# Kernel tuning notes

Measured on AMD Instinct MI355X. Metric: run time of the kernel, lower is better.

Reference implementation:

```python
import jax, jax.numpy as jnp
import numpy as np

V = 6890            # FAUST mesh vertices (also n_classes of the dense head)
C_IN = 3            # raw xyz signal
R, A = 5, 8         # kernel_size = (n_radial, n_angular)
ROT_DELTA = 1
ROTS = tuple(range(0, A, ROT_DELTA))  # 8 rotations
DIMS = [100, 100, 100]
EPS_BN = 1e-3       # keras BatchNormalization default epsilon


def setup_inputs() -> dict:
    key = jax.random.key(0)
    ks = jax.random.split(key, 12)
    inp = {}
    inp["signal"] = jax.random.normal(ks[0], (V, C_IN), jnp.float32)
    inp["bc_idx"] = jax.random.randint(ks[1], (V, R, A, 3), 0, V, dtype=jnp.int32)
    w = jax.random.uniform(ks[2], (V, R, A, 3), jnp.float32)
    inp["bc_w"] = w / jnp.sum(w, axis=-1, keepdims=True)  # convex barycentric weights
    # keras Normalization (not adapted): mean=0, var=1
    inp["norm_mean"] = jnp.zeros((C_IN,), jnp.float32)
    inp["norm_var"] = jnp.ones((C_IN,), jnp.float32)
    # ConvDirac templates: (amt_templates, n_radial, n_angular, c_in) + bias
    cins = [C_IN] + DIMS[:-1]
    for i, (ci, t) in enumerate(zip(cins, DIMS)):
        inp[f"w{i}"] = jax.random.normal(ks[3 + i], (t, R, A, ci), jnp.float32) * 0.05
        inp[f"b{i}"] = jnp.zeros((t,), jnp.float32)
    # BatchNorm (inference mode) params, stacked over the 3 blocks
    inp["bn_gamma"] = jnp.ones((3, DIMS[0]), jnp.float32)
    inp["bn_beta"] = jnp.zeros((3, DIMS[0]), jnp.float32)
    inp["bn_mean"] = jax.random.normal(ks[6], (3, DIMS[0]), jnp.float32) * 0.01
    inp["bn_var"] = jnp.ones((3, DIMS[0]), jnp.float32)
    inp["dense_w"] = jax.random.normal(ks[7], (DIMS[-1], V), jnp.float32) * 0.02
    inp["dense_b"] = jnp.zeros((V,), jnp.float32)
    return inp


def _isc_dirac(sig, bc_idx, bc_w, W, b):
    """Intrinsic surface conv (Dirac): barycentric patch gather + multi-rotation fold.
    sig: (V, C); bc_idx/bc_w: (V, R, A, 3); W: (T, R, A, C); b: (T,)
    returns (V, n_rot, T) after relu."""
    # patch operator: interpolate signal at template vertices -> (V, R, A, C)
    patch = jnp.einsum('vraic,vrai->vrac', sig[bc_idx], bc_w)
    # rotate the (small) template over the angular axis instead of the patch
    Wrot = jnp.stack([jnp.roll(W, -r, axis=2) for r in ROTS])  # (n_rot, T, R, A, C)
    out = jnp.einsum('vrac,ntrac->vnt', patch, Wrot) + b
    return jax.nn.relu(out)


def _amp(x):
    """AngularMaxPooling: keep the rotation response with max L2 norm. x: (V, n_rot, T)."""
    idx = jnp.argmax(jnp.linalg.norm(x, axis=-1), axis=-1)  # (V,)
    return jnp.take_along_axis(x, idx[:, None, None], axis=1)[:, 0, :]


def _bn(x, g, b, m, v):
    return g * (x - m) * jax.lax.rsqrt(v + EPS_BN) + b


def reference(signal, bc_idx, bc_w, norm_mean, norm_var, w0, b0, w1, b1, w2, b2,
              bn_gamma, bn_beta, bn_mean, bn_var, dense_w, dense_b):
    x = (signal - norm_mean) / jnp.sqrt(norm_var)
    for i, (W, b) in enumerate(((w0, b0), (w1, b1), (w2, b2))):
        x = _isc_dirac(x, bc_idx, bc_w, W, b)      # (V, n_rot, T)
        x = _amp(x)                                 # (V, T)
        x = _bn(x, bn_gamma[i], bn_beta[i], bn_mean[i], bn_var[i])
        # dropout: identity at inference
    return x @ dense_w + dense_b                    # (V, 6890)
```

## Files before the change

kernel.cpp:

```cpp
#include <hip/hip_runtime.h>

#define VN 6890
#define TN 100
#define NOUT 800
#define MP 6912
#define NP 896

typedef __attribute__((ext_vector_type(8))) short bf16x8;
typedef __attribute__((ext_vector_type(4))) float f32x4;

__device__ __forceinline__ unsigned short f2bf(float f) {
    unsigned u = __float_as_uint(f);
    return (unsigned short)((u + 0x7FFFu + ((u >> 16) & 1u)) >> 16);
}
__device__ __forceinline__ void split_bf16(float f, short* h, short* l) {
    unsigned short hb = f2bf(f);
    float hf = __uint_as_float(((unsigned)hb) << 16);
    *h = (short)hb;
    *l = (short)f2bf(f - hf);
}
__device__ __forceinline__ void gload16(const short* g, void* lds) {
    __builtin_amdgcn_global_load_lds(
        (const __attribute__((address_space(1))) void*)g,
        (__attribute__((address_space(3))) void*)lds, 16, 0, 0);
}

__global__ __launch_bounds__(256) void norm_kernel(
    const float* __restrict__ sig, const float* __restrict__ mean,
    const float* __restrict__ var, float* __restrict__ x0)
{
    int i = blockIdx.x * blockDim.x + threadIdx.x;
    if (i < VN * 3) {
        int c = i % 3;
        x0[i] = (sig[i] - mean[c]) / sqrtf(var[c]);
    }
}

template<int CIN, int KPAD>
__global__ __launch_bounds__(256) void rotw_split(
    const float* __restrict__ W, short* __restrict__ Bh, short* __restrict__ Bl)
{
    const int n = blockIdx.x;
    const int K = 40 * CIN;
    const int rot = n / TN, t = n - rot * TN;
    for (int k = threadIdx.x; k < KPAD; k += 256) {
        float w = 0.f;
        if (n < NOUT && k < K) {
            int ra = k / CIN, c = k - ra * CIN;
            int r = ra >> 3, a = ra & 7;
            int a2 = (a + rot) & 7;
            w = W[((t * 5 + r) * 8 + a2) * CIN + c];
        }
        short h, l; split_bf16(w, &h, &l);
        Bh[(size_t)n * KPAD + k] = h;
        Bl[(size_t)n * KPAD + k] = l;
    }
}

template<int CIN, int KPAD>
__global__ __launch_bounds__(256) void patch_split(
    const float* __restrict__ x, const int* __restrict__ bidx,
    const float* __restrict__ bw, short* __restrict__ Ph, short* __restrict__ Pl)
{
    __shared__ int   sIdx[120];
    __shared__ float sW[120];
    const int v = blockIdx.x;
    const int tid = threadIdx.x;
    const int K = 40 * CIN;
    if (v >= VN) {
        for (int e = tid; e < KPAD; e += 256) {
            Ph[(size_t)v * KPAD + e] = 0;
            Pl[(size_t)v * KPAD + e] = 0;
        }
        return;
    }
    if (tid < 120) { sIdx[tid] = bidx[v * 120 + tid]; sW[tid] = bw[v * 120 + tid]; }
    __syncthreads();
    for (int e = tid; e < KPAD; e += 256) {
        float s = 0.f;
        if (e < K) {
            int ra = e / CIN, c = e - ra * CIN;
            s = sW[ra * 3 + 0] * x[sIdx[ra * 3 + 0] * CIN + c]
              + sW[ra * 3 + 1] * x[sIdx[ra * 3 + 1] * CIN + c]
              + sW[ra * 3 + 2] * x[sIdx[ra * 3 + 2] * CIN + c];
        }
        short h, l; split_bf16(s, &h, &l);
        Ph[(size_t)v * KPAD + e] = h;
        Pl[(size_t)v * KPAD + e] = l;
    }
}

template<bool CONV_EPI>
__global__ __launch_bounds__(256, 2) void mfma_gemm(
    const short* __restrict__ Ah, const short* __restrict__ Al,
    const short* __restrict__ Bh, const short* __restrict__ Bl,
    const float* __restrict__ bias, float* __restrict__ C,
    int M, int N, int ldc, int K)
{
    __shared__ __align__(16) short AhS[4096];
    __shared__ __align__(16) short AlS[4096];
    __shared__ __align__(16) short BhS[4096];
    __shared__ __align__(16) short BlS[4096];

    const int tid  = threadIdx.x;
    const int wave = tid >> 6;
    const int lane = tid & 63;
    const int lr = lane & 15, lg = lane >> 4;
    const int wm = wave >> 1, wn = wave & 1;
    const int m0 = blockIdx.x * 128;
    const int n0 = blockIdx.y * 128;

    const int off0 = tid * 16, off1 = off0 + 4096;
    const int row0 = off0 >> 6, row1 = off1 >> 6;
    const int g0 = ((off0 >> 4) & 3) ^ ((row0 >> 1) & 3);
    const int g1 = ((off1 >> 4) & 3) ^ ((row1 >> 1) & 3);
    const size_t aO0 = (size_t)(m0 + row0) * K + g0 * 8;
    const size_t aO1 = (size_t)(m0 + row1) * K + g1 * 8;
    const size_t bO0 = (size_t)(n0 + row0) * K + g0 * 8;
    const size_t bO1 = (size_t)(n0 + row1) * K + g1 * 8;
    const int wofs = wave << 10;

    int aRd[4], bRd[4];
    #pragma unroll
    for (int f = 0; f < 4; ++f) {
        int ar = wm * 64 + f * 16 + lr;
        aRd[f] = ar * 64 + ((lg ^ ((ar >> 1) & 3)) << 4);
        int br = wn * 64 + f * 16 + lr;
        bRd[f] = br * 64 + ((lg ^ ((br >> 1) & 3)) << 4);
    }

    f32x4 acc[4][4];
    #pragma unroll
    for (int i = 0; i < 4; ++i)
        #pragma unroll
        for (int j = 0; j < 4; ++j)
            acc[i][j] = (f32x4){0.f, 0.f, 0.f, 0.f};

    const int nkt = K >> 5;
    for (int kt = 0; kt < nkt; ++kt) {
        const int k0 = kt << 5;
        gload16(Ah + aO0 + k0, (char*)AhS + wofs);
        gload16(Ah + aO1 + k0, (char*)AhS + 4096 + wofs);
        gload16(Al + aO0 + k0, (char*)AlS + wofs);
        gload16(Al + aO1 + k0, (char*)AlS + 4096 + wofs);
        gload16(Bh + bO0 + k0, (char*)BhS + wofs);
        gload16(Bh + bO1 + k0, (char*)BhS + 4096 + wofs);
        gload16(Bl + bO0 + k0, (char*)BlS + wofs);
        gload16(Bl + bO1 + k0, (char*)BlS + 4096 + wofs);
        __syncthreads();

        bf16x8 ah[4], al[4], bh[4], bl[4];
        #pragma unroll
        for (int f = 0; f < 4; ++f) {
            ah[f] = *(const bf16x8*)((const char*)AhS + aRd[f]);
            al[f] = *(const bf16x8*)((const char*)AlS + aRd[f]);
            bh[f] = *(const bf16x8*)((const char*)BhS + bRd[f]);
            bl[f] = *(const bf16x8*)((const char*)BlS + bRd[f]);
        }
        #pragma unroll
        for (int i = 0; i < 4; ++i)
            #pragma unroll
            for (int j = 0; j < 4; ++j)
                acc[i][j] = __builtin_amdgcn_mfma_f32_16x16x32_bf16(ah[i], bh[j], acc[i][j], 0, 0, 0);
        #pragma unroll
        for (int i = 0; i < 4; ++i)
            #pragma unroll
            for (int j = 0; j < 4; ++j)
                acc[i][j] = __builtin_amdgcn_mfma_f32_16x16x32_bf16(ah[i], bl[j], acc[i][j], 0, 0, 0);
        #pragma unroll
        for (int i = 0; i < 4; ++i)
            #pragma unroll
            for (int j = 0; j < 4; ++j)
                acc[i][j] = __builtin_amdgcn_mfma_f32_16x16x32_bf16(al[i], bh[j], acc[i][j], 0, 0, 0);
        __syncthreads();
    }

    #pragma unroll
    for (int i = 0; i < 4; ++i) {
        const int mb = m0 + wm * 64 + i * 16 + lg * 4;
        #pragma unroll
        for (int j = 0; j < 4; ++j) {
            const int n = n0 + wn * 64 + j * 16 + lr;
            if (CONV_EPI) {
                const float bv = bias[n % TN];
                #pragma unroll
                for (int q = 0; q < 4; ++q)
                    C[(size_t)(mb + q) * ldc + n] = fmaxf(acc[i][j][q] + bv, 0.f);
            } else {
                if (n < N) {
                    const float bv = bias[n];
                    #pragma unroll
                    for (int q = 0; q < 4; ++q)
                        if (mb + q < M)
                            C[(size_t)(mb + q) * ldc + n] = acc[i][j][q] + bv;
                }
            }
        }
    }
}

template<bool CONV_EPI>
__global__ __launch_bounds__(256, 4) void tile_gemm(
    const float* __restrict__ A, const float* __restrict__ B,
    const float* __restrict__ bias, float* __restrict__ C,
    int M, int N, int K)
{
    __shared__ __align__(16) float As[32][132];
    __shared__ __align__(16) float Bs[32][68];

    const int tid = threadIdx.x;
    const int m0 = blockIdx.x * 128;
    const int n0 = blockIdx.y * 64;
    const int ty = tid >> 4;
    const int tx = tid & 15;
    const int nkt = (K + 31) >> 5;

    float4 aR[4];
    float2 bR[4];

    auto load_tile = [&](int kt) {
        const int k0 = kt << 5;
        #pragma unroll
        for (int j = 0; j < 4; ++j) {
            int q = tid + 256 * j;
            int row = q >> 3, kq = (q & 7) << 2;
            int v = m0 + row, k = k0 + kq;
            if (v < M && k < K)
                aR[j] = *reinterpret_cast<const float4*>(A + (size_t)v * K + k);
            else
                aR[j] = make_float4(0.f, 0.f, 0.f, 0.f);
        }
        #pragma unroll
        for (int j = 0; j < 2; ++j) {
            int q = tid + 256 * j;
            int krow = q >> 4, nq = (q & 15) << 2;
            int k = k0 + krow, n = n0 + nq;
            bR[2 * j]     = (k < K && n + 1 < N)
                ? *reinterpret_cast<const float2*>(B + (size_t)k * N + n)     : make_float2(0.f, 0.f);
            bR[2 * j + 1] = (k < K && n + 3 < N)
                ? *reinterpret_cast<const float2*>(B + (size_t)k * N + n + 2) : make_float2(0.f, 0.f);
        }
    };
    auto stage = [&]() {
        #pragma unroll
        for (int j = 0; j < 4; ++j) {
            int q = tid + 256 * j;
            int row = q >> 3, kq = (q & 7) << 2;
            As[kq + 0][row] = aR[j].x; As[kq + 1][row] = aR[j].y;
            As[kq + 2][row] = aR[j].z; As[kq + 3][row] = aR[j].w;
        }
        #pragma unroll
        for (int j = 0; j < 2; ++j) {
            int q = tid + 256 * j;
            int krow = q >> 4, nq = (q & 15) << 2;
            *reinterpret_cast<float2*>(&Bs[krow][nq])     = bR[2 * j];
            *reinterpret_cast<float2*>(&Bs[krow][nq + 2]) = bR[2 * j + 1];
        }
    };

    float acc[8][4];
    #pragma unroll
    for (int i = 0; i < 8; ++i)
        #pragma unroll
        for (int j = 0; j < 4; ++j) acc[i][j] = 0.f;

    load_tile(0);
    stage();
    __syncthreads();

    for (int kt = 0; kt < nkt; ++kt) {
        if (kt + 1 < nkt) load_tile(kt + 1);
        #pragma unroll 16
        for (int k = 0; k < 32; ++k) {
            float4 a0 = *reinterpret_cast<const float4*>(&As[k][ty * 8]);
            float4 a1 = *reinterpret_cast<const float4*>(&As[k][ty * 8 + 4]);
            float4 b  = *reinterpret_cast<const float4*>(&Bs[k][tx * 4]);
            float av[8] = {a0.x, a0.y, a0.z, a0.w, a1.x, a1.y, a1.z, a1.w};
            float bv[4] = {b.x, b.y, b.z, b.w};
            #pragma unroll
            for (int i = 0; i < 8; ++i)
                #pragma unroll
                for (int j = 0; j < 4; ++j)
                    acc[i][j] = fmaf(av[i], bv[j], acc[i][j]);
        }
        __syncthreads();
        if (kt + 1 < nkt) { stage(); __syncthreads(); }
    }

    #pragma unroll
    for (int i = 0; i < 8; ++i) {
        int vr = m0 + ty * 8 + i;
        if (vr >= M) continue;
        int nb = n0 + tx * 4;
        size_t base = (size_t)vr * N + nb;
        if (nb + 1 < N) {
            float2 o = {acc[i][0] + bias[nb], acc[i][1] + bias[nb + 1]};
            *reinterpret_cast<float2*>(C + base) = o;
        }
        if (nb + 3 < N) {
            float2 o = {acc[i][2] + bias[nb + 2], acc[i][3] + bias[nb + 3]};
            *reinterpret_cast<float2*>(C + base + 2) = o;
        }
    }
}

__global__ __launch_bounds__(256) void amp_bn(
    const float* __restrict__ conv,
    const float* __restrict__ g,  const float* __restrict__ be,
    const float* __restrict__ mu, const float* __restrict__ var,
    float* __restrict__ xout)
{
    int v = blockIdx.x * 4 + (threadIdx.x >> 6);
    int lane = threadIdx.x & 63;
    if (v >= VN) return;
    const float* y = conv + (size_t)v * NP;

    float s[8];
    #pragma unroll
    for (int n = 0; n < 8; ++n) {
        float t1 = y[n * TN + lane];
        float t2 = (lane < 36) ? y[n * TN + 64 + lane] : 0.f;
        s[n] = t1 * t1 + t2 * t2;
    }
    #pragma unroll
    for (int off = 32; off > 0; off >>= 1)
        #pragma unroll
        for (int n = 0; n < 8; ++n) s[n] += __shfl_xor(s[n], off);

    int best = 0; float bs = s[0];
    #pragma unroll
    for (int n = 1; n < 8; ++n) { if (s[n] > bs) { bs = s[n]; best = n; } }

    const float* yb = y + best * TN;
    for (int t = lane; t < TN; t += 64) {
        float inv = 1.0f / sqrtf(var[t] + 1e-3f);
        xout[v * TN + t] = g[t] * (yb[t] - mu[t]) * inv + be[t];
    }
}

__global__ __launch_bounds__(256) void dense_a_split(
    const float* __restrict__ xA, short* __restrict__ Ah, short* __restrict__ Al)
{
    int i = blockIdx.x * 256 + threadIdx.x;
    if (i >= MP * 128) return;
    int v = i >> 7, k = i & 127;
    float f = (v < VN && k < TN) ? xA[v * TN + k] : 0.f;
    short h, l; split_bf16(f, &h, &l);
    Ah[i] = h; Al[i] = l;
}
__global__ __launch_bounds__(256) void dense_b_split(
    const float* __restrict__ dw, short* __restrict__ Bh, short* __restrict__ Bl)
{
    int i = blockIdx.x * 256 + threadIdx.x;
    if (i >= MP * 128) return;
    int n = i >> 7, k = i & 127;
    float f = (n < VN && k < TN) ? dw[(size_t)k * VN + n] : 0.f;
    short h, l; split_bf16(f, &h, &l);
    Bh[i] = h; Bl[i] = l;
}

extern "C" void kernel_launch(void* const* d_in, const int* in_sizes, int n_in,
                              void* d_out, int out_size, void* d_ws, size_t ws_size,
                              hipStream_t stream) {
    const float* signal = (const float*)d_in[0];
    const int*   bcix   = (const int*)  d_in[1];
    const float* bcw    = (const float*)d_in[2];
    const float* nmean  = (const float*)d_in[3];
    const float* nvar   = (const float*)d_in[4];
    const float* w0     = (const float*)d_in[5];
    const float* b0     = (const float*)d_in[6];
    const float* w1     = (const float*)d_in[7];
    const float* b1     = (const float*)d_in[8];
    const float* w2     = (const float*)d_in[9];
    const float* b2     = (const float*)d_in[10];
    const float* bng    = (const float*)d_in[11];
    const float* bnb    = (const float*)d_in[12];
    const float* bnm    = (const float*)d_in[13];
    const float* bnv    = (const float*)d_in[14];
    const float* dw     = (const float*)d_in[15];
    const float* db     = (const float*)d_in[16];
    float* out = (float*)d_out;

    float* x0 = (float*)d_ws;
    float* xA = x0 + 20736;
    float* xB = xA + 689024;
    short* dAh = (short*)xB;
    short* dAl = dAh + (size_t)MP * 128;
    short* dBh = dAl + (size_t)MP * 128;
    short* dBl = dBh + (size_t)MP * 128;
    const size_t ws_need = (size_t)709760 * 4 + (size_t)4 * MP * 128 * 2;
    const bool dense_mfma = ws_size >= ws_need;

    short* Ph  = (short*)out;
    short* Pl  = Ph  + (size_t)MP * 4000;
    short* Bth = Pl  + (size_t)MP * 4000;
    short* Btl = Bth + (size_t)NP * 4000;
    float* conv = out + (size_t)MP * 4000 + (size_t)NP * 4000;

    dim3 cgrid(MP / 128, NP / 128);
    dim3 mgrid(MP / 128, MP / 128);
    dim3 dgrid((VN + 127) / 128, (VN + 63) / 64);
    int ampg = (VN + 3) / 4;

    norm_kernel<<<(VN * 3 + 255) / 256, 256, 0, stream>>>(signal, nmean, nvar, x0);

    rotw_split<3, 128><<<NP, 256, 0, stream>>>(w0, Bth, Btl);
    patch_split<3, 128><<<MP, 256, 0, stream>>>(x0, bcix, bcw, Ph, Pl);
    mfma_gemm<true><<<cgrid, 256, 0, stream>>>(Ph, Pl, Bth, Btl, b0, conv, VN, NOUT, NP, 128);
    amp_bn<<<ampg, 256, 0, stream>>>(conv, bng, bnb, bnm, bnv, xA);

    rotw_split<100, 4000><<<NP, 256, 0, stream>>>(w1, Bth, Btl);
    patch_split<100, 4000><<<MP, 256, 0, stream>>>(xA, bcix, bcw, Ph, Pl);
    mfma_gemm<true><<<cgrid, 256, 0, stream>>>(Ph, Pl, Bth, Btl, b1, conv, VN, NOUT, NP, 4000);
    amp_bn<<<ampg, 256, 0, stream>>>(conv, bng + 100, bnb + 100, bnm + 100, bnv + 100, xB);

    rotw_split<100, 4000><<<NP, 256, 0, stream>>>(w2, Bth, Btl);
    patch_split<100, 4000><<<MP, 256, 0, stream>>>(xB, bcix, bcw, Ph, Pl);
    mfma_gemm<true><<<cgrid, 256, 0, stream>>>(Ph, Pl, Bth, Btl, b2, conv, VN, NOUT, NP, 4000);
    amp_bn<<<ampg, 256, 0, stream>>>(conv, bng + 200, bnb + 200, bnm + 200, bnv + 200, xA);

    if (dense_mfma) {
        dense_a_split<<<(MP * 128 + 255) / 256, 256, 0, stream>>>(xA, dAh, dAl);
        dense_b_split<<<(MP * 128 + 255) / 256, 256, 0, stream>>>(dw, dBh, dBl);
        mfma_gemm<false><<<mgrid, 256, 0, stream>>>(dAh, dAl, dBh, dBl, db, out, VN, VN, VN, 128);
    } else {
        tile_gemm<false><<<dgrid, 256, 0, stream>>>(xA, dw, db, out, VN, VN, TN);
    }
}
```

Baseline: 758.5 us.

## Split-K the conv GEMMs in two and fold bias/relu into AMP kernel

Splits the K dimension of the ISC conv GEMMs across two z-slices, each writing a separate partial conv buffer. The bias add and ReLU move into amp_bn, which sums the two partials before the norm/argmax. amp_bn also keeps all rotation values in registers, so it no longer re-reads the chosen rotation from memory. The aim is to double the block count (54x7 was too few for the CUs on the long-K layers), at the cost of writing and reading a second fp32 conv buffer. The second buffer must fit in the output scratch region.

```diff
diff --git a/kernel.cpp b/kernel.cpp
--- a/kernel.cpp
+++ b/kernel.cpp
@@ -5,6 +5,7 @@
 #define NOUT 800
 #define MP 6912
 #define NP 896
+#define CONVSZ (MP * NP)
 
 typedef __attribute__((ext_vector_type(8))) short bf16x8;
 typedef __attribute__((ext_vector_type(4))) float f32x4;
@@ -95,7 +96,7 @@
     const short* __restrict__ Ah, const short* __restrict__ Al,
     const short* __restrict__ Bh, const short* __restrict__ Bl,
     const float* __restrict__ bias, float* __restrict__ C,
-    int M, int N, int ldc, int K)
+    int M, int N, int ldc, int K, int Ksl, int cstride)
 {
     __shared__ __align__(16) short AhS[4096];
     __shared__ __align__(16) short AlS[4096];
@@ -109,15 +110,18 @@
     const int wm = wave >> 1, wn = wave & 1;
     const int m0 = blockIdx.x * 128;
     const int n0 = blockIdx.y * 128;
+    const int kbase = blockIdx.z * Ksl;
+    const int kcnt  = min(Ksl, K - kbase);
+    if (CONV_EPI) C += (size_t)blockIdx.z * cstride;
 
     const int off0 = tid * 16, off1 = off0 + 4096;
     const int row0 = off0 >> 6, row1 = off1 >> 6;
     const int g0 = ((off0 >> 4) & 3) ^ ((row0 >> 1) & 3);
     const int g1 = ((off1 >> 4) & 3) ^ ((row1 >> 1) & 3);
-    const size_t aO0 = (size_t)(m0 + row0) * K + g0 * 8;
-    const size_t aO1 = (size_t)(m0 + row1) * K + g1 * 8;
-    const size_t bO0 = (size_t)(n0 + row0) * K + g0 * 8;
-    const size_t bO1 = (size_t)(n0 + row1) * K + g1 * 8;
+    const size_t aO0 = (size_t)(m0 + row0) * K + kbase + g0 * 8;
+    const size_t aO1 = (size_t)(m0 + row1) * K + kbase + g1 * 8;
+    const size_t bO0 = (size_t)(n0 + row0) * K + kbase + g0 * 8;
+    const size_t bO1 = (size_t)(n0 + row1) * K + kbase + g1 * 8;
     const int wofs = wave << 10;
 
     int aRd[4], bRd[4];
@@ -136,7 +140,7 @@
         for (int j = 0; j < 4; ++j)
             acc[i][j] = (f32x4){0.f, 0.f, 0.f, 0.f};
 
-    const int nkt = K >> 5;
+    const int nkt = kcnt >> 5;
     for (int kt = 0; kt < nkt; ++kt) {
         const int k0 = kt << 5;
         gload16(Ah + aO0 + k0, (char*)AhS + wofs);
@@ -182,10 +186,9 @@
         for (int j = 0; j < 4; ++j) {
             const int n = n0 + wn * 64 + j * 16 + lr;
             if (CONV_EPI) {
-                const float bv = bias[n % TN];
                 #pragma unroll
                 for (int q = 0; q < 4; ++q)
-                    C[(size_t)(mb + q) * ldc + n] = fmaxf(acc[i][j][q] + bv, 0.f);
+                    C[(size_t)(mb + q) * ldc + n] = acc[i][j][q];
             } else {
                 if (n < N) {
                     const float bv = bias[n];
@@ -306,6 +309,7 @@
 
 __global__ __launch_bounds__(256) void amp_bn(
     const float* __restrict__ conv,
+    const float* __restrict__ bias,
     const float* __restrict__ g,  const float* __restrict__ be,
     const float* __restrict__ mu, const float* __restrict__ var,
     float* __restrict__ xout)
@@ -313,14 +317,20 @@
     int v = blockIdx.x * 4 + (threadIdx.x >> 6);
     int lane = threadIdx.x & 63;
     if (v >= VN) return;
-    const float* y = conv + (size_t)v * NP;
-
-    float s[8];
+    const float* y0 = conv + (size_t)v * NP;
+    const float* y1 = y0 + CONVSZ;
+
+    const float bLo = bias[lane];
+    const float bHi = (lane < 36) ? bias[64 + lane] : 0.f;
+
+    float t1[8], t2[8], s[8];
     #pragma unroll
     for (int n = 0; n < 8; ++n) {
-        float t1 = y[n * TN + lane];
-        float t2 = (lane < 36) ? y[n * TN + 64 + lane] : 0.f;
-        s[n] = t1 * t1 + t2 * t2;
+        float a = fmaxf(y0[n * TN + lane] + y1[n * TN + lane] + bLo, 0.f);
+        float b = (lane < 36)
+            ? fmaxf(y0[n * TN + 64 + lane] + y1[n * TN + 64 + lane] + bHi, 0.f) : 0.f;
+        t1[n] = a; t2[n] = b;
+        s[n] = a * a + b * b;
     }
     #pragma unroll
     for (int off = 32; off > 0; off >>= 1)
@@ -331,10 +341,18 @@
     #pragma unroll
     for (int n = 1; n < 8; ++n) { if (s[n] > bs) { bs = s[n]; best = n; } }
 
-    const float* yb = y + best * TN;
-    for (int t = lane; t < TN; t += 64) {
+    float a = t1[0], b = t2[0];
+    #pragma unroll
+    for (int n = 1; n < 8; ++n) { if (best == n) { a = t1[n]; b = t2[n]; } }
+
+    {
+        float inv = 1.0f / sqrtf(var[lane] + 1e-3f);
+        xout[v * TN + lane] = g[lane] * (a - mu[lane]) * inv + be[lane];
+    }
+    if (lane < 36) {
+        int t = 64 + lane;
         float inv = 1.0f / sqrtf(var[t] + 1e-3f);
-        xout[v * TN + t] = g[t] * (yb[t] - mu[t]) * inv + be[t];
+        xout[v * TN + t] = g[t] * (b - mu[t]) * inv + be[t];
     }
 }
 
@@ -397,8 +415,8 @@
     short* Btl = Bth + (size_t)NP * 4000;
     float* conv = out + (size_t)MP * 4000 + (size_t)NP * 4000;
 
-    dim3 cgrid(MP / 128, NP / 128);
-    dim3 mgrid(MP / 128, MP / 128);
+    dim3 cgrid(MP / 128, NP / 128, 2);
+    dim3 mgrid(MP / 128, MP / 128, 1);
     dim3 dgrid((VN + 127) / 128, (VN + 63) / 64);
     int ampg = (VN + 3) / 4;
 
@@ -406,23 +424,23 @@
 
     rotw_split<3, 128><<<NP, 256, 0, stream>>>(w0, Bth, Btl);
     patch_split<3, 128><<<MP, 256, 0, stream>>>(x0, bcix, bcw, Ph, Pl);
-    mfma_gemm<true><<<cgrid, 256, 0, stream>>>(Ph, Pl, Bth, Btl, b0, conv, VN, NOUT, NP, 128);
-    amp_bn<<<ampg, 256, 0, stream>>>(conv, bng, bnb, bnm, bnv, xA);
+    mfma_gemm<true><<<cgrid, 256, 0, stream>>>(Ph, Pl, Bth, Btl, b0, conv, VN, NOUT, NP, 128, 64, CONVSZ);
+    amp_bn<<<ampg, 256, 0, stream>>>(conv, b0, bng, bnb, bnm, bnv, xA);
 
     rotw_split<100, 4000><<<NP, 256, 0, stream>>>(w1, Bth, Btl);
     patch_split<100, 4000><<<MP, 256, 0, stream>>>(xA, bcix, bcw, Ph, Pl);
-    mfma_gemm<true><<<cgrid, 256, 0, stream>>>(Ph, Pl, Bth, Btl, b1, conv, VN, NOUT, NP, 4000);
-    amp_bn<<<ampg, 256, 0, stream>>>(conv, bng + 100, bnb + 100, bnm + 100, bnv + 100, xB);
+    mfma_gemm<true><<<cgrid, 256, 0, stream>>>(Ph, Pl, Bth, Btl, b1, conv, VN, NOUT, NP, 4000, 2016, CONVSZ);
+    amp_bn<<<ampg, 256, 0, stream>>>(conv, b1, bng + 100, bnb + 100, bnm + 100, bnv + 100, xB);
 
     rotw_split<100, 4000><<<NP, 256, 0, stream>>>(w2, Bth, Btl);
     patch_split<100, 4000><<<MP, 256, 0, stream>>>(xB, bcix, bcw, Ph, Pl);
-    mfma_gemm<true><<<cgrid, 256, 0, stream>>>(Ph, Pl, Bth, Btl, b2, conv, VN, NOUT, NP, 4000);
-    amp_bn<<<ampg, 256, 0, stream>>>(conv, bng + 200, bnb + 200, bnm + 200, bnv + 200, xA);
+    mfma_gemm<true><<<cgrid, 256, 0, stream>>>(Ph, Pl, Bth, Btl, b2, conv, VN, NOUT, NP, 4000, 2016, CONVSZ);
+    amp_bn<<<ampg, 256, 0, stream>>>(conv, b2, bng + 200, bnb + 200, bnm + 200, bnv + 200, xA);
 
     if (dense_mfma) {
         dense_a_split<<<(MP * 128 + 255) / 256, 256, 0, stream>>>(xA, dAh, dAl);
         dense_b_split<<<(MP * 128 + 255) / 256, 256, 0, stream>>>(dw, dBh, dBl);
-        mfma_gemm<false><<<mgrid, 256, 0, stream>>>(dAh, dAl, dBh, dBl, db, out, VN, VN, VN, 128);
+        mfma_gemm<false><<<mgrid, 256, 0, stream>>>(dAh, dAl, dBh, dBl, db, out, VN, VN, VN, 128, 128, 0);
     } else {
         tile_gemm<false><<<dgrid, 256, 0, stream>>>(xA, dw, db, out, VN, VN, TN);
     }
```

After: 756.3 us. No clear change (-0.3%).
